# Kernel tuning notes

Measured on AMD Instinct MI355X. Metric: run time of the kernel, lower is better.

Reference implementation:

```python
import jax, jax.numpy as jnp
import numpy as np

N_NODES = 50000
N_EDGES = 1600000
IN_DIM = 128
OUT_DIM = 16
N_HEADS = 8


def setup_inputs() -> dict:
    key = jax.random.key(0)
    ks = jax.random.split(key, 9)
    s = 1.0 / np.sqrt(IN_DIM)
    return {
        "h": jax.random.normal(ks[0], (N_NODES, IN_DIM), jnp.float32),
        "Wq": jax.random.normal(ks[1], (IN_DIM, OUT_DIM * N_HEADS), jnp.float32) * s,
        "bq": jax.random.normal(ks[2], (OUT_DIM * N_HEADS,), jnp.float32) * 0.01,
        "Wk": jax.random.normal(ks[3], (IN_DIM, OUT_DIM * N_HEADS), jnp.float32) * s,
        "bk": jax.random.normal(ks[4], (OUT_DIM * N_HEADS,), jnp.float32) * 0.01,
        "Wv": jax.random.normal(ks[5], (IN_DIM, OUT_DIM * N_HEADS), jnp.float32) * s,
        "bv": jax.random.normal(ks[6], (OUT_DIM * N_HEADS,), jnp.float32) * 0.01,
        "src": jax.random.randint(ks[7], (N_EDGES,), 0, N_NODES, jnp.int32),
        "dst": jax.random.randint(ks[8], (N_EDGES,), 0, N_NODES, jnp.int32),
    }


def reference(h, Wq, bq, Wk, bk, Wv, bv, src, dst):
    n_nodes = h.shape[0]
    # node-wise Q/K/V projections -> [N, H, D]
    Q = (h @ Wq + bq).reshape(n_nodes, N_HEADS, OUT_DIM)
    K = (h @ Wk + bk).reshape(n_nodes, N_HEADS, OUT_DIM)
    V = (h @ Wv + bv).reshape(n_nodes, N_HEADS, OUT_DIM)
    # edge-wise score: (K[src] * Q[dst]).sum(-1), scaled-exp with clamp
    score = jnp.sum(K[src] * Q[dst], axis=-1)  # [E, H]
    score = jnp.exp(jnp.clip(score / np.sqrt(OUT_DIM), -5.0, 5.0))
    # scatter-sum weighted values and normalizers to dst nodes
    msg = V[src] * score[:, :, None]  # [E, H, D]
    wV = jax.ops.segment_sum(msg, dst, num_segments=n_nodes)  # [N, H, D]
    z = jax.ops.segment_sum(score, dst, num_segments=n_nodes)  # [N, H]
    return wV / (z[:, :, None] + 1e-6)
```

## Files before the change

### kernel.cpp

```cpp
#include <hip/hip_runtime.h>
#include <hip/hip_bf16.h>
#include <cstddef>

#define N_NODES 50000
#define N_EDGES 1600000
#define IN_DIM 128
#define OUT_DIM 16
#define N_HEADS 8
#define QKV_DIM 128
#define HS_STRIDE 136

#define SUBB 3125
#define GCAP 768
#define BH_CHUNK 8192
#define BH_BLOCKS 196
#define GEMM_M 32
#define GEMM_BLOCKS 1563
#define FUSED_BLOCKS (BH_BLOCKS + GEMM_BLOCKS)

typedef __hip_bfloat16 bf16;
typedef short bf16x8 __attribute__((ext_vector_type(8)));
typedef float f32x4  __attribute__((ext_vector_type(4)));

__device__ __forceinline__ float b2f(bf16 x) { return __bfloat162float(x); }

__device__ __forceinline__ float u16tof(unsigned int u) {
    unsigned int x = u << 16;
    float f;
    __builtin_memcpy(&f, &x, 4);
    return f;
}

__device__ __forceinline__ unsigned short f2bf(float v) {
    bf16 b = __float2bfloat16(v);
    unsigned short u;
    __builtin_memcpy(&u, &b, 2);
    return u;
}

__global__ __launch_bounds__(256) void sentinel_kernel(unsigned short* __restrict__ out, int n) {
    int i = blockIdx.x * 256 + threadIdx.x;
    if (i < n) out[i] = 0x42C8;
}

__global__ __launch_bounds__(256) void prep_kernel(
    const unsigned short* __restrict__ hraw,
    const void* __restrict__ Wqr, const void* __restrict__ bqr,
    const void* __restrict__ Wkr, const void* __restrict__ bkr,
    const void* __restrict__ Wvr, const void* __restrict__ bvr,
    int* __restrict__ flag,
    unsigned short* __restrict__ Wfrag, float* __restrict__ bias_f,
    int* __restrict__ gcur)
{
    __shared__ int red[256];
    const int t   = threadIdx.x;
    const int tid = blockIdx.x * 256 + t;

    for (int i = tid; i < SUBB; i += 24 * 256) gcur[i] = 0;

    int cnt = 0;
    for (int i = t; i < 8192; i += 256) {
        unsigned short u = hraw[i];
        int e = (u >> 7) & 0xFF;
        if (e == 0xFF || e > 0x85 || (e == 0 && (u & 0x7F) != 0)) cnt++;
    }
    red[t] = cnt;
    __syncthreads();
    for (int s = 128; s > 0; s >>= 1) {
        if (t < s) red[t] += red[t + s];
        __syncthreads();
    }
    const bool f32 = (red[0] > 100);
    if (blockIdx.x == 0 && t == 0) *flag = red[0];

    if (tid < 384) {
        int mat = tid >> 7, c = tid & 127;
        const void* bp = (mat == 0) ? bqr : (mat == 1) ? bkr : bvr;
        bias_f[tid] = f32 ? ((const float*)bp)[c] : b2f(((const bf16*)bp)[c]);
    }

    int l  = tid & 63;
    int s  = (tid >> 6) & 3;
    int nt = tid >> 8;
    int n  = nt * 16 + (l & 15);
    int k0 = s * 32 + (l >> 4) * 8;
    int mat = n >> 7, c = n & 127;
    const void* Wp = (mat == 0) ? Wqr : (mat == 1) ? Wkr : Wvr;

    unsigned short v[8];
#pragma unroll
    for (int j = 0; j < 8; ++j) {
        int k = k0 + j;
        float w = f32 ? ((const float*)Wp)[k * QKV_DIM + c]
                      : b2f(((const bf16*)Wp)[k * QKV_DIM + c]);
        v[j] = f2bf(w);
    }
    ushort4* o = (ushort4*)(Wfrag + (size_t)tid * 8);
    o[0] = make_ushort4(v[0], v[1], v[2], v[3]);
    o[1] = make_ushort4(v[4], v[5], v[6], v[7]);
}

__global__ __launch_bounds__(256) void fused_gs_kernel(
    const void* __restrict__ hraw,
    const unsigned short* __restrict__ Wfrag, const float* __restrict__ bias_f,
    const int* __restrict__ flag,
    unsigned short* __restrict__ Qt, unsigned short* __restrict__ KVt,
    const int* __restrict__ src, const int* __restrict__ dst,
    unsigned int* __restrict__ gpacked, int* __restrict__ gcur)
{
    __shared__ __align__(16) unsigned char arena[12544];
    const int t = threadIdx.x;

    if (blockIdx.x < BH_BLOCKS) {
        int* lcnt = (int*)arena;

        const int b    = blockIdx.x;
        const int base = b * BH_CHUNK;
        const int nb   = min(N_EDGES - base, BH_CHUNK);

        for (int i = t; i < SUBB; i += 256) lcnt[i] = 0;
        __syncthreads();

        for (int i = t; i < nb; i += 256)
            atomicAdd(&lcnt[dst[base + i] >> 4], 1);
        __syncthreads();

        for (int i = t; i < SUBB; i += 256) {
            int c = lcnt[i];
            if (c) lcnt[i] = i * GCAP + atomicAdd(&gcur[i], c);
        }
        __syncthreads();

        for (int i = t; i < nb; i += 256) {
            int d  = dst[base + i];
            int bk = d >> 4;
            int pos = atomicAdd(&lcnt[bk], 1);
            if (pos < (bk + 1) * GCAP)
                gpacked[pos] = (unsigned int)src[base + i] | ((unsigned int)(d & 15) << 16);
        }

    } else {
        unsigned short* smem = (unsigned short*)arena;

        const bool f32 = (*flag > 100);
        const int m0 = (blockIdx.x - BH_BLOCKS) * GEMM_M;

#pragma unroll
        for (int it = 0; it < 4; ++it) {
            int idx = it * 1024 + t * 4;
            int r = idx >> 7, k = idx & 127;
            int row = m0 + r;
            ushort4 w4 = make_ushort4(0, 0, 0, 0);
            if (row < N_NODES) {
                if (f32) {
                    float4 v4 = ((const float4*)hraw)[(size_t)row * 32 + (k >> 2)];
                    w4 = make_ushort4(f2bf(v4.x), f2bf(v4.y), f2bf(v4.z), f2bf(v4.w));
                } else {
                    uint2 u = ((const uint2*)hraw)[(size_t)row * 32 + (k >> 2)];
                    w4 = make_ushort4((unsigned short)(u.x & 0xffffu), (unsigned short)(u.x >> 16),
                                      (unsigned short)(u.y & 0xffffu), (unsigned short)(u.y >> 16));
                }
            }
            *(ushort4*)&smem[r * HS_STRIDE + k] = w4;
        }
        __syncthreads();

        const int lane = t & 63;
        const int wave = t >> 6;
        const int qd   = lane >> 4;
        const int ln15 = lane & 15;

        bf16x8 afr[2][4];
#pragma unroll
        for (int ms = 0; ms < 2; ++ms)
#pragma unroll
            for (int s = 0; s < 4; ++s)
                afr[ms][s] = *(const bf16x8*)&smem[(ms * 16 + ln15) * HS_STRIDE + s * 32 + qd * 8];

        __syncthreads();

#pragma unroll
        for (int p = 0; p < 3; ++p) {
#pragma unroll
            for (int ii = 0; ii < 2; ++ii) {
                const int i   = 2 * p + ii;
                const int nt  = wave + i * 4;
                const int col = nt * 16 + ln15;
                const float bs = bias_f[col];
                const int c127 = col & 127;

                bf16x8 bfr[4];
#pragma unroll
                for (int s = 0; s < 4; ++s)
                    bfr[s] = *(const bf16x8*)(Wfrag + ((size_t)(nt * 4 + s) * 64 + lane) * 8);

#pragma unroll
                for (int ms = 0; ms < 2; ++ms) {
                    f32x4 acc = {0.f, 0.f, 0.f, 0.f};
#pragma unroll
                    for (int s = 0; s < 4; ++s)
                        acc = __builtin_amdgcn_mfma_f32_16x16x32_bf16(afr[ms][s], bfr[s], acc, 0, 0, 0);
#pragma unroll
                    for (int r = 0; r < 4; ++r) {
                        int rl = ms * 16 + qd * 4 + r;
                        smem[rl * HS_STRIDE + c127] = f2bf(acc[r] + bs);
                    }
                }
            }
            __syncthreads();
            if (p == 0) {
                for (int q = t; q < 512; q += 256) {
                    int row = q >> 4, c = q & 15;
                    int grow = m0 + row;
                    if (grow < N_NODES)
                        ((uint4*)Qt)[grow * 16 + c] = *(const uint4*)&smem[row * HS_STRIDE + c * 8];
                }
            } else {
                for (int q = t; q < 1024; q += 256) {
                    int row = q >> 5, g = q & 31;
                    int grow = m0 + row;
                    if (grow < N_NODES)
                        ((uint2*)KVt)[(size_t)grow * 64 + g * 2 + (p - 1)] =
                            *(const uint2*)&smem[row * HS_STRIDE + g * 4];
                }
            }
            __syncthreads();
        }
    }
}

__global__ __launch_bounds__(256) void bucket_agg_kernel(
    const unsigned short* __restrict__ Qt, const unsigned short* __restrict__ KVt,
    const unsigned int* __restrict__ gpacked, const int* __restrict__ gcur,
    const int* __restrict__ flag, void* __restrict__ out)
{
    __shared__ unsigned int   lds_pk[GCAP];
    __shared__ unsigned short lds_src[GCAP];
    __shared__ int cnt16[16], base16[16], cur16[16];
    __shared__ int n_s;

    const int sb = blockIdx.x;
    const int t  = threadIdx.x;

    if (t < 16) { cnt16[t] = 0; cur16[t] = 0; }
    if (t == 0) n_s = min(gcur[sb], GCAP);
    __syncthreads();
    const int n  = n_s;
    const int gb = sb * GCAP;

    for (int j = t; j < n; j += 256) {
        unsigned int pk = gpacked[gb + j];
        lds_pk[j] = pk;
        atomicAdd(&cnt16[(pk >> 16) & 15], 1);
    }
    __syncthreads();
    if (t == 0) {
        int acc = 0;
#pragma unroll
        for (int i = 0; i < 16; ++i) { base16[i] = acc; acc += cnt16[i]; }
    }
    __syncthreads();
    for (int j = t; j < n; j += 256) {
        unsigned int pk = lds_pk[j];
        int dl = (pk >> 16) & 15;
        int pos = base16[dl] + atomicAdd(&cur16[dl], 1);
        lds_src[pos] = (unsigned short)(pk & 0xffffu);
    }
    __syncthreads();

    const int wave = t >> 6;
    const int lane = t & 63;
    const int half = lane >> 5;
    const int hl   = lane & 31;
    const uint4* KV4 = (const uint4*)KVt;
    const bool of32 = (*flag > 100);

    for (int dl = wave; dl < 16; dl += 4) {
        const int d = sb * 16 + dl;
        uint2 qw = ((const uint2*)Qt)[d * 32 + hl];
        const float q0 = u16tof(qw.x & 0xffffu), q1 = u16tof(qw.x >> 16);
        const float q2 = u16tof(qw.y & 0xffffu), q3 = u16tof(qw.y >> 16);
        const int off = base16[dl];
        const int nd  = cnt16[dl];

        float a0 = 0.f, a1 = 0.f, a2 = 0.f, a3 = 0.f, zz = 0.f;

#define CONSUME(KV, SCMASK)                                                     \
        {                                                                       \
            float p = fmaf(u16tof((KV).x & 0xffffu), q0,                        \
                      fmaf(u16tof((KV).x >> 16), q1,                            \
                      fmaf(u16tof((KV).y & 0xffffu), q2,                        \
                           u16tof((KV).y >> 16) * q3)));                        \
            p += __shfl_xor(p, 1);                                              \
            p += __shfl_xor(p, 2);                                              \
            float sc = __expf(__builtin_amdgcn_fmed3f(p * 0.25f, -5.f, 5.f));   \
            sc *= (SCMASK);                                                     \
            a0 = fmaf(u16tof((KV).z & 0xffffu), sc, a0);                        \
            a1 = fmaf(u16tof((KV).z >> 16),     sc, a1);                        \
            a2 = fmaf(u16tof((KV).w & 0xffffu), sc, a2);                        \
            a3 = fmaf(u16tof((KV).w >> 16),     sc, a3);                        \
            zz += sc;                                                           \
        }

        int j = 0;
        for (; j + 8 <= nd; j += 8) {
            int e[4];
#pragma unroll
            for (int u = 0; u < 4; ++u) e[u] = lds_src[off + j + 2 * u + half];
            uint4 kv[4];
#pragma unroll
            for (int u = 0; u < 4; ++u) kv[u] = KV4[e[u] * 32 + hl];
#pragma unroll
            for (int u = 0; u < 4; ++u) CONSUME(kv[u], 1.f)
        }
        for (; j + 2 <= nd; j += 2) {
            int e = lds_src[off + j + half];
            uint4 kv = KV4[e * 32 + hl];
            CONSUME(kv, 1.f)
        }
        if (j < nd) {
            int e = lds_src[off + j];
            uint4 kv = KV4[e * 32 + hl];
            CONSUME(kv, (half == 0) ? 1.f : 0.f)
        }
#undef CONSUME

        a0 += __shfl_xor(a0, 32);
        a1 += __shfl_xor(a1, 32);
        a2 += __shfl_xor(a2, 32);
        a3 += __shfl_xor(a3, 32);
        zz += __shfl_xor(zz, 32);

        const float inv = 1.f / (zz + 1e-6f);
        const float r0 = a0 * inv, r1 = a1 * inv, r2 = a2 * inv, r3 = a3 * inv;

        if (half == 0) {
            if (of32) {
                ((float4*)out)[d * 32 + hl] = make_float4(r0, r1, r2, r3);
            } else {
                unsigned int w0 = ((unsigned int)f2bf(r1) << 16) | f2bf(r0);
                unsigned int w1 = ((unsigned int)f2bf(r3) << 16) | f2bf(r2);
                ((uint2*)out)[d * 32 + hl] = make_uint2(w0, w1);
            }
        }
    }
}

extern "C" void kernel_launch(void* const* d_in, const int* in_sizes, int n_in,
                              void* d_out, int out_size, void* d_ws, size_t ws_size,
                              hipStream_t stream)
{
    const void* h  = d_in[0];
    const void* Wq = d_in[1];
    const void* bq = d_in[2];
    const void* Wk = d_in[3];
    const void* bk = d_in[4];
    const void* Wv = d_in[5];
    const void* bv = d_in[6];
    const int*  src = (const int*)d_in[7];
    const int*  dst = (const int*)d_in[8];

    const size_t NQ = (size_t)N_NODES * QKV_DIM;
    const size_t WFRAG_N = 24 * 4 * 64 * 8;
    const size_t GPACK_N = (size_t)SUBB * GCAP;

    const size_t need = 3 * NQ * 2 + WFRAG_N * 2 + 384 * 4 + 64
                      + (size_t)SUBB * 4 + 64 + GPACK_N * 4;

    if (ws_size < need) {
        sentinel_kernel<<<(out_size + 255) / 256, 256, 0, stream>>>((unsigned short*)d_out, out_size);
        return;
    }

    unsigned short* Qt  = (unsigned short*)d_ws;
    unsigned short* KVt = Qt + NQ;
    unsigned short* Wfrag = KVt + 2 * NQ;
    float* bias_f = (float*)(Wfrag + WFRAG_N);
    int* flag     = (int*)(bias_f + 384);
    int* gcur     = flag + 16;
    unsigned int* gpacked = (unsigned int*)(gcur + SUBB + 11);

    prep_kernel<<<24, 256, 0, stream>>>((const unsigned short*)h,
        Wq, bq, Wk, bk, Wv, bv, flag, Wfrag, bias_f, gcur);

    fused_gs_kernel<<<FUSED_BLOCKS, 256, 0, stream>>>(h, Wfrag, bias_f, flag,
        Qt, KVt, src, dst, gpacked, gcur);

    bucket_agg_kernel<<<SUBB, 256, 0, stream>>>(Qt, KVt, gpacked, gcur, flag, d_out);
}
```

Baseline: 269.5 us.

## Double the GEMM row tile and software-pipeline KV gathers in aggregation

The projection GEMM now handles 64 rows per block instead of 32, halving the number of GEMM blocks and reusing each loaded weight fragment across twice as many MFMA row tiles, at the cost of more LDS and registers. The aggregation loop now prefetches the next group of four gathered KV vectors before consuming the current group, so gather latency overlaps with the score/exp/accumulate math. This raises register pressure and may lower occupancy.

```diff
diff --git a/kernel.cpp b/kernel.cpp
--- a/kernel.cpp
+++ b/kernel.cpp
@@ -14,8 +14,8 @@
 #define GCAP 768
 #define BH_CHUNK 8192
 #define BH_BLOCKS 196
-#define GEMM_M 32
-#define GEMM_BLOCKS 1563
+#define GEMM_M 64
+#define GEMM_BLOCKS 782
 #define FUSED_BLOCKS (BH_BLOCKS + GEMM_BLOCKS)
 
 typedef __hip_bfloat16 bf16;
@@ -108,7 +108,7 @@
     const int* __restrict__ src, const int* __restrict__ dst,
     unsigned int* __restrict__ gpacked, int* __restrict__ gcur)
 {
-    __shared__ __align__(16) unsigned char arena[12544];
+    __shared__ __align__(16) unsigned char arena[GEMM_M * HS_STRIDE * 2];
     const int t = threadIdx.x;
 
     if (blockIdx.x < BH_BLOCKS) {
@@ -146,7 +146,7 @@
         const int m0 = (blockIdx.x - BH_BLOCKS) * GEMM_M;
 
 #pragma unroll
-        for (int it = 0; it < 4; ++it) {
+        for (int it = 0; it < 8; ++it) {
             int idx = it * 1024 + t * 4;
             int r = idx >> 7, k = idx & 127;
             int row = m0 + r;
@@ -170,9 +170,9 @@
         const int qd   = lane >> 4;
         const int ln15 = lane & 15;
 
-        bf16x8 afr[2][4];
-#pragma unroll
-        for (int ms = 0; ms < 2; ++ms)
+        bf16x8 afr[4][4];
+#pragma unroll
+        for (int ms = 0; ms < 4; ++ms)
 #pragma unroll
             for (int s = 0; s < 4; ++s)
                 afr[ms][s] = *(const bf16x8*)&smem[(ms * 16 + ln15) * HS_STRIDE + s * 32 + qd * 8];
@@ -195,7 +195,7 @@
                     bfr[s] = *(const bf16x8*)(Wfrag + ((size_t)(nt * 4 + s) * 64 + lane) * 8);
 
 #pragma unroll
-                for (int ms = 0; ms < 2; ++ms) {
+                for (int ms = 0; ms < 4; ++ms) {
                     f32x4 acc = {0.f, 0.f, 0.f, 0.f};
 #pragma unroll
                     for (int s = 0; s < 4; ++s)
@@ -209,14 +209,14 @@
             }
             __syncthreads();
             if (p == 0) {
-                for (int q = t; q < 512; q += 256) {
+                for (int q = t; q < 1024; q += 256) {
                     int row = q >> 4, c = q & 15;
                     int grow = m0 + row;
                     if (grow < N_NODES)
                         ((uint4*)Qt)[grow * 16 + c] = *(const uint4*)&smem[row * HS_STRIDE + c * 8];
                 }
             } else {
-                for (int q = t; q < 1024; q += 256) {
+                for (int q = t; q < 2048; q += 256) {
                     int row = q >> 5, g = q & 31;
                     int grow = m0 + row;
                     if (grow < N_NODES)
@@ -303,15 +303,31 @@
         }
 
         int j = 0;
-        for (; j + 8 <= nd; j += 8) {
-            int e[4];
-#pragma unroll
-            for (int u = 0; u < 4; ++u) e[u] = lds_src[off + j + 2 * u + half];
-            uint4 kv[4];
-#pragma unroll
-            for (int u = 0; u < 4; ++u) kv[u] = KV4[e[u] * 32 + hl];
-#pragma unroll
-            for (int u = 0; u < 4; ++u) CONSUME(kv[u], 1.f)
+        const int full = nd & ~7;
+        if (full > 0) {
+            uint4 kvA[4];
+            {
+                int eA[4];
+#pragma unroll
+                for (int u = 0; u < 4; ++u) eA[u] = lds_src[off + 2 * u + half];
+#pragma unroll
+                for (int u = 0; u < 4; ++u) kvA[u] = KV4[eA[u] * 32 + hl];
+            }
+            for (j = 0; j + 8 < full; j += 8) {
+                int eB[4];
+#pragma unroll
+                for (int u = 0; u < 4; ++u) eB[u] = lds_src[off + j + 8 + 2 * u + half];
+                uint4 kvB[4];
+#pragma unroll
+                for (int u = 0; u < 4; ++u) kvB[u] = KV4[eB[u] * 32 + hl];
+#pragma unroll
+                for (int u = 0; u < 4; ++u) CONSUME(kvA[u], 1.f)
+#pragma unroll
+                for (int u = 0; u < 4; ++u) kvA[u] = kvB[u];
+            }
+#pragma unroll
+            for (int u = 0; u < 4; ++u) CONSUME(kvA[u], 1.f)
+            j = full;
         }
         for (; j + 2 <= nd; j += 2) {
             int e = lds_src[off + j + half];
```

After: 267.2 us. About the same (-0.8%).
